# Kernel optimization log

Hardware: AMD Instinct MI355X
Metric: run time of the kernel (lower is better)

The kernel has to match this reference:

```python
import jax, jax.numpy as jnp
import numpy as np

NUM_HEAD = 16


def setup_inputs() -> dict:
    key = jax.random.key(0)
    k1, k2, k3 = jax.random.split(key, 3)
    E = 1024
    x = jax.random.normal(k1, (4, 2048, E), dtype=jnp.float32)
    W1 = jax.random.normal(k2, (E, 3 * E), dtype=jnp.float32) * 0.02
    b1 = jnp.zeros((3 * E,), dtype=jnp.float32)
    W2 = jax.random.normal(k3, (E, E), dtype=jnp.float32) * 0.02
    b2 = jnp.zeros((E,), dtype=jnp.float32)
    return {"x": x, "W1": W1, "b1": b1, "W2": W2, "b2": b2}


def reference(x, W1, b1, W2, b2):
    # Fused QKV projection: (n, s, 3E)
    h = x @ W1 + b1
    n, s, _ = h.shape
    # Split into heads FIRST (matches torch reshape), then transpose: (n, H, s, 3*d_head)
    h = h.reshape(n, s, NUM_HEAD, -1).transpose(0, 2, 1, 3)
    # Chunk last dim into q, k, v: each (n, H, s, d_head)
    q, k, v = jnp.split(h, 3, axis=-1)
    dk = jnp.asarray(v.shape[-1], x.dtype) ** 0.5
    # Naive full S x S attention (faithful to source)
    w = jnp.einsum("nhqd,nhkd->nhqk", q, k) / dk
    w = jax.nn.softmax(w, axis=-1)  # dropout1 is identity at eval
    att = jnp.einsum("nhqk,nhkd->nhqd", w, v)
    att = att.transpose(0, 2, 1, 3).reshape(n, s, -1)  # (n, s, E)
    return att @ W2 + b2  # dropout2 identity at eval
```

## Files before the change

kernel.cpp:

```cpp
#include <hip/hip_runtime.h>
#include <math.h>
#include <stdint.h>
#include <stddef.h>


#define SEQ    2048
#define NB     4
#define E_DIM  1024
#define N1     3072
#define M_TOK  8192
#define NHEAD  16
#define DHEAD  64

typedef __attribute__((ext_vector_type(4))) float    floatx4;
typedef __attribute__((ext_vector_type(8))) short    shortx8;
typedef __attribute__((ext_vector_type(4))) unsigned short ushortx4;

__device__ __forceinline__ unsigned short f2bf(float f) {
    union { float f; unsigned u; } v; v.f = f;
    unsigned r = (v.u + 0x7FFFu + ((v.u >> 16) & 1u)) >> 16;
    return (unsigned short)r;
}
__device__ __forceinline__ unsigned fbits(float f) {
    union { float f; unsigned u; } v; v.f = f; return v.u;
}
__device__ __forceinline__ float bitsf(unsigned u) {
    union { unsigned u; float f; } v; v.u = u; return v.f;
}

__device__ __forceinline__ void gl_lds16(const void* g, void* l) {
    __builtin_amdgcn_global_load_lds(
        (const __attribute__((address_space(1))) unsigned int*)g,
        (__attribute__((address_space(3))) unsigned int*)l, 16, 0, 0);
}

__global__ __launch_bounds__(256) void cvt_bf16(
    const float* __restrict__ in, unsigned short* __restrict__ out)
{
    const size_t i = ((size_t)blockIdx.x * 256 + threadIdx.x) * 8;
    float4 a = *(const float4*)(in + i);
    float4 b = *(const float4*)(in + i + 4);
    ushortx4 o0 = { f2bf(a.x), f2bf(a.y), f2bf(a.z), f2bf(a.w) };
    ushortx4 o1 = { f2bf(b.x), f2bf(b.y), f2bf(b.z), f2bf(b.w) };
    *(ushortx4*)(out + i)     = o0;
    *(ushortx4*)(out + i + 4) = o1;
}

__global__ __launch_bounds__(256) void cvt_transpose(
    const float* __restrict__ W, unsigned short* __restrict__ Wt, int K, int N)
{
    __shared__ unsigned short tile[32][33];
    const int tx = threadIdx.x, ty = threadIdx.y;
    const int n0 = blockIdx.x * 32, k0 = blockIdx.y * 32;
#pragma unroll
    for (int r = 0; r < 4; ++r) {
        const int k = ty + r * 8;
        tile[tx][k] = f2bf(W[(size_t)(k0 + k) * N + n0 + tx]);
    }
    __syncthreads();
#pragma unroll
    for (int r = 0; r < 4; ++r) {
        const int n = ty + r * 8;
        Wt[(size_t)(n0 + n) * K + k0 + tx] = tile[n][tx];
    }
}

template <bool OUT_BF16, bool FUSE>
__global__ __launch_bounds__(256) void gemm_bf16(
    const short* __restrict__ A, const short* __restrict__ Bt,
    const float* __restrict__ bias, void* __restrict__ Cout,
    unsigned short* __restrict__ Vt,
    int M, int N, int K)
{
    __shared__ short As[128 * 32];
    __shared__ short Bs[128 * 32];

    const int t    = threadIdx.x;
    const int lane = t & 63, w = t >> 6;
    const int quad = lane >> 4, l15 = lane & 15;
    const int bm = blockIdx.y * 128, bn = blockIdx.x * 128;
    const int m0w = (w >> 1) * 64, n0w = (w & 1) * 64;

    const int lrow = lane >> 2;
    const int lcol = (lane & 3) * 8;
    const short* Ag0 = A  + (size_t)(bm + (2 * w + 0) * 16 + lrow) * K + lcol;
    const short* Ag1 = A  + (size_t)(bm + (2 * w + 1) * 16 + lrow) * K + lcol;
    const short* Bg0 = Bt + (size_t)(bn + (2 * w + 0) * 16 + lrow) * K + lcol;
    const short* Bg1 = Bt + (size_t)(bn + (2 * w + 1) * 16 + lrow) * K + lcol;
    short* Al0 = As + (2 * w + 0) * 512;
    short* Al1 = As + (2 * w + 1) * 512;
    short* Bl0 = Bs + (2 * w + 0) * 512;
    short* Bl1 = Bs + (2 * w + 1) * 512;

    floatx4 acc[4][4];
#pragma unroll
    for (int i = 0; i < 4; ++i)
#pragma unroll
        for (int j = 0; j < 4; ++j) acc[i][j] = (floatx4)0.f;

    for (int k0 = 0; k0 < K; k0 += 32) {
        __syncthreads();
        gl_lds16(Ag0, Al0); gl_lds16(Ag1, Al1);
        gl_lds16(Bg0, Bl0); gl_lds16(Bg1, Bl1);
        Ag0 += 32; Ag1 += 32; Bg0 += 32; Bg1 += 32;
        __syncthreads();

        shortx8 af[4], bf[4];
#pragma unroll
        for (int mi = 0; mi < 4; ++mi)
            af[mi] = *(const shortx8*)(As + (m0w + mi * 16 + l15) * 32 + quad * 8);
#pragma unroll
        for (int ni = 0; ni < 4; ++ni)
            bf[ni] = *(const shortx8*)(Bs + (n0w + ni * 16 + l15) * 32 + quad * 8);
#pragma unroll
        for (int mi = 0; mi < 4; ++mi)
#pragma unroll
            for (int ni = 0; ni < 4; ++ni)
                acc[mi][ni] = __builtin_amdgcn_mfma_f32_16x16x32_bf16(
                    af[mi], bf[ni], acc[mi][ni], 0, 0, 0);
    }

    float bv[4];
#pragma unroll
    for (int ni = 0; ni < 4; ++ni) bv[ni] = bias[bn + n0w + ni * 16 + l15];

#pragma unroll
    for (int ni = 0; ni < 4; ++ni) {
        const int col   = bn + n0w + ni * 16 + l15;
        const int cm    = col % 192;
        const int vhead = col / 192;
#pragma unroll
        for (int mi = 0; mi < 4; ++mi) {
            const int row0 = bm + m0w + mi * 16 + quad * 4;
            float v[4];
#pragma unroll
            for (int r = 0; r < 4; ++r) v[r] = acc[mi][ni][r] + bv[ni];
            if (OUT_BF16) {
                if (FUSE && cm < DHEAD) {
#pragma unroll
                    for (int r = 0; r < 4; ++r) v[r] *= 0.125f;
                }
                unsigned short* H = (unsigned short*)Cout;
#pragma unroll
                for (int r = 0; r < 4; ++r)
                    H[(size_t)(row0 + r) * N + col] = f2bf(v[r]);
                if (FUSE && cm >= 2 * DHEAD) {
                    const int nb = row0 >> 11;
                    const int s  = row0 & 2047;
                    const int d  = cm - 2 * DHEAD;
                    ushortx4 pk = { f2bf(v[0]), f2bf(v[1]), f2bf(v[2]), f2bf(v[3]) };
                    *(ushortx4*)(Vt + ((size_t)(nb * NHEAD + vhead) * DHEAD + d) * SEQ + s) = pk;
                }
            } else {
                float* C = (float*)Cout;
#pragma unroll
                for (int r = 0; r < 4; ++r)
                    C[(size_t)(row0 + r) * N + col] = v[r];
            }
        }
    }
}

__global__ __launch_bounds__(256, 3) void attn_mfma(
    const short* __restrict__ h, const short* __restrict__ Vt,
    unsigned short* __restrict__ att)
{
    __shared__ short Ks[64 * 64];
    __shared__ short Vs[64 * 64];
    __shared__ short Pl[4][64 * 64];
    __shared__ float Ls[4][64];

    const int t    = threadIdx.x;
    const int lane = t & 63, w = t >> 6;
    const int quad = lane >> 4, l15 = lane & 15;
    const int r7   = l15 & 7;
    const int bh = blockIdx.x, n = bh >> 4, head = bh & 15;
    const int q0 = blockIdx.y * 256 + w * 64;

    const short* hQ  = h + (size_t)n * SEQ * N1 + head * (3 * DHEAD);
    const short* hK  = hQ + DHEAD;
    const short* Vtb = Vt + (size_t)bh * DHEAD * SEQ;

    const int srow = t >> 2;
    const int sc0  = (t & 3) * 2;
    const int sk   = srow & 7;
    const short* gK = hK  + (size_t)srow * N1  + sc0 * 8;
    const short* gV = Vtb + (size_t)srow * SEQ + sc0 * 8;
    short* lK0 = Ks + srow * 64 + ((sc0    ) ^ sk) * 8;
    short* lK1 = Ks + srow * 64 + ((sc0 + 1) ^ sk) * 8;
    short* lV0 = Vs + srow * 64 + ((sc0    ) ^ sk) * 8;
    short* lV1 = Vs + srow * 64 + ((sc0 + 1) ^ sk) * 8;

    shortx8 qf[4][2];
#pragma unroll
    for (int qt = 0; qt < 4; ++qt)
#pragma unroll
        for (int kt = 0; kt < 2; ++kt)
            qf[qt][kt] = *(const shortx8*)(hQ + (size_t)(q0 + qt * 16 + l15) * N1
                                           + kt * 32 + quad * 8);

    floatx4 O[4][4];
    float lsum[4];
#pragma unroll
    for (int mi = 0; mi < 4; ++mi) {
        lsum[mi] = 0.f;
#pragma unroll
        for (int nt = 0; nt < 4; ++nt) O[mi][nt] = (floatx4)0.f;
    }

    int4 ka = *(const int4*)gK, kb = *(const int4*)(gK + 8);
    int4 va = *(const int4*)gV, vb = *(const int4*)(gV + 8);

    short* Pw = Pl[w];

    for (int kv0 = 0; kv0 < SEQ; kv0 += 64) {
        __syncthreads();
        *(int4*)lK0 = ka;
        *(int4*)lK1 = kb;
        *(int4*)lV0 = va;
        *(int4*)lV1 = vb;
        __syncthreads();
        if (kv0 + 64 < SEQ) {
            const short* gKn = gK + (size_t)(kv0 + 64) * N1;
            const short* gVn = gV + (kv0 + 64);
            ka = *(const int4*)gKn; kb = *(const int4*)(gKn + 8);
            va = *(const int4*)gVn; vb = *(const int4*)(gVn + 8);
        }

#pragma unroll
        for (int kvt = 0; kvt < 4; ++kvt) {
            const short* krow = Ks + (kvt * 16 + l15) * 64;
            shortx8 kf0 = *(const shortx8*)(krow + ((quad ^ r7) * 8));
            shortx8 kf1 = *(const shortx8*)(krow + (((quad ^ r7) ^ 4) * 8));
            floatx4 s[4];
#pragma unroll
            for (int qt = 0; qt < 4; ++qt) {
                s[qt] = __builtin_amdgcn_mfma_f32_16x16x32_bf16(
                    kf0, qf[qt][0], (floatx4)0.f, 0, 0, 0);
                s[qt] = __builtin_amdgcn_mfma_f32_16x16x32_bf16(
                    kf1, qf[qt][1], s[qt], 0, 0, 0);
            }
#pragma unroll
            for (int qt = 0; qt < 4; ++qt) {
                const float p0 = __expf(s[qt][0]);
                const float p1 = __expf(s[qt][1]);
                const float p2 = __expf(s[qt][2]);
                const float p3 = __expf(s[qt][3]);
                const unsigned d01 = __builtin_amdgcn_perm(fbits(p1), fbits(p0), 0x07060302u);
                const unsigned d23 = __builtin_amdgcn_perm(fbits(p3), fbits(p2), 0x07060302u);
                lsum[qt] += bitsf(d01 << 16) + bitsf(d01 & 0xFFFF0000u)
                          + bitsf(d23 << 16) + bitsf(d23 & 0xFFFF0000u);
                uint2 pk = { d01, d23 };
                *(uint2*)(Pw + (qt * 16 + l15) * 64
                          + ((2 * kvt + (quad >> 1)) ^ r7) * 8 + (quad & 1) * 4) = pk;
            }
        }

#pragma unroll
        for (int kt2 = 0; kt2 < 2; ++kt2) {
            const int coff = (((kt2 * 4 + quad) ^ r7)) * 8;
            shortx8 pf[4], vf[4];
#pragma unroll
            for (int mi = 0; mi < 4; ++mi)
                pf[mi] = *(const shortx8*)(Pw + (mi * 16 + l15) * 64 +
                                           (((kt2 * 4 + quad) ^ r7)) * 8);
#pragma unroll
            for (int nt = 0; nt < 4; ++nt)
                vf[nt] = *(const shortx8*)(Vs + (nt * 16 + l15) * 64 + coff);
#pragma unroll
            for (int mi = 0; mi < 4; ++mi)
#pragma unroll
                for (int nt = 0; nt < 4; ++nt)
                    O[mi][nt] = __builtin_amdgcn_mfma_f32_16x16x32_bf16(
                        pf[mi], vf[nt], O[mi][nt], 0, 0, 0);
        }
    }

#pragma unroll
    for (int qt = 0; qt < 4; ++qt) {
        lsum[qt] += __shfl_xor(lsum[qt], 16);
        lsum[qt] += __shfl_xor(lsum[qt], 32);
    }
    if (quad == 0) {
#pragma unroll
        for (int qt = 0; qt < 4; ++qt) Ls[w][qt * 16 + l15] = lsum[qt];
    }

#pragma unroll
    for (int mi = 0; mi < 4; ++mi)
#pragma unroll
        for (int r = 0; r < 4; ++r) {
            const int   ql  = mi * 16 + quad * 4 + r;
            const float inv = 1.f / Ls[w][ql];
            const size_t row = (size_t)n * SEQ + q0 + ql;
#pragma unroll
            for (int nt = 0; nt < 4; ++nt)
                att[row * E_DIM + head * DHEAD + nt * 16 + l15] =
                    f2bf(O[mi][nt][r] * inv);
        }
}

extern "C" void kernel_launch(void* const* d_in, const int* in_sizes, int n_in,
                              void* d_out, int out_size, void* d_ws, size_t ws_size,
                              hipStream_t stream)
{
    const float* x  = (const float*)d_in[0];
    const float* W1 = (const float*)d_in[1];
    const float* b1 = (const float*)d_in[2];
    const float* W2 = (const float*)d_in[3];
    const float* b2 = (const float*)d_in[4];
    float* out = (float*)d_out;

    char* ws = (char*)d_ws;
    unsigned short* x_bf  = (unsigned short*)(ws);
    unsigned short* W1t   = (unsigned short*)(ws + (16u << 20));
    unsigned short* W2t   = (unsigned short*)(ws + (22u << 20));
    unsigned short* h_bf  = (unsigned short*)(ws + (24u << 20));
    unsigned short* attb  = (unsigned short*)(ws + (72u << 20));
    unsigned short* Vtw   = (unsigned short*)(ws + (88u << 20));

    cvt_bf16<<<dim3((M_TOK * E_DIM) / (256 * 8)), 256, 0, stream>>>(x, x_bf);
    cvt_transpose<<<dim3(N1 / 32, E_DIM / 32), dim3(32, 8), 0, stream>>>(W1, W1t, E_DIM, N1);
    cvt_transpose<<<dim3(E_DIM / 32, E_DIM / 32), dim3(32, 8), 0, stream>>>(W2, W2t, E_DIM, E_DIM);

    gemm_bf16<true, true><<<dim3(N1 / 128, M_TOK / 128), 256, 0, stream>>>(
        (const short*)x_bf, (const short*)W1t, b1, h_bf, Vtw, M_TOK, N1, E_DIM);

    attn_mfma<<<dim3(NB * NHEAD, SEQ / 256), 256, 0, stream>>>(
        (const short*)h_bf, (const short*)Vtw, attb);

    gemm_bf16<false, false><<<dim3(E_DIM / 128, M_TOK / 128), 256, 0, stream>>>(
        (const short*)attb, (const short*)W2t, b2, out, nullptr, M_TOK, E_DIM, E_DIM);
}
```

Before: 301.3 us.

## Shrink attention blocks to two waves and use native exp2 with folded scale

The attention kernel now runs 128-thread blocks covering 128 queries instead of 256. This doubles the grid and halves the LDS used per block, but each thread now stages four 16-byte K and V chunks instead of two. Softmax exponentials switch to the hardware exp2 builtin, with log2(e) folded into the Q pre-scale in the QKV GEMM epilogue, which removes a multiply per exp. The trade-off is that K/V tile staging is now shared by fewer waves, so each wave does more global-to-LDS traffic, and register pressure rises from the larger prefetch buffers.

```diff
diff --git a/kernel.cpp b/kernel.cpp
--- a/kernel.cpp
+++ b/kernel.cpp
@@ -15,6 +15,12 @@
 typedef __attribute__((ext_vector_type(4))) float    floatx4;
 typedef __attribute__((ext_vector_type(8))) short    shortx8;
 typedef __attribute__((ext_vector_type(4))) unsigned short ushortx4;
+
+#if __has_builtin(__builtin_amdgcn_exp2f)
+#define EXP2(x) __builtin_amdgcn_exp2f(x)
+#else
+#define EXP2(x) __expf((x) * 0.6931471805599453f)
+#endif
 
 __device__ __forceinline__ unsigned short f2bf(float f) {
     union { float f; unsigned u; } v; v.f = f;
@@ -138,7 +144,7 @@
             if (OUT_BF16) {
                 if (FUSE && cm < DHEAD) {
 #pragma unroll
-                    for (int r = 0; r < 4; ++r) v[r] *= 0.125f;
+                    for (int r = 0; r < 4; ++r) v[r] *= 0.18033688011112042f;
                 }
                 unsigned short* H = (unsigned short*)Cout;
 #pragma unroll
@@ -161,35 +167,33 @@
     }
 }
 
-__global__ __launch_bounds__(256, 3) void attn_mfma(
+__global__ __launch_bounds__(128, 2) void attn_mfma(
     const short* __restrict__ h, const short* __restrict__ Vt,
     unsigned short* __restrict__ att)
 {
     __shared__ short Ks[64 * 64];
     __shared__ short Vs[64 * 64];
-    __shared__ short Pl[4][64 * 64];
-    __shared__ float Ls[4][64];
+    __shared__ short Pl[2][64 * 64];
+    __shared__ float Ls[2][64];
 
     const int t    = threadIdx.x;
     const int lane = t & 63, w = t >> 6;
     const int quad = lane >> 4, l15 = lane & 15;
     const int r7   = l15 & 7;
     const int bh = blockIdx.x, n = bh >> 4, head = bh & 15;
-    const int q0 = blockIdx.y * 256 + w * 64;
+    const int q0 = blockIdx.y * 128 + w * 64;
 
     const short* hQ  = h + (size_t)n * SEQ * N1 + head * (3 * DHEAD);
     const short* hK  = hQ + DHEAD;
     const short* Vtb = Vt + (size_t)bh * DHEAD * SEQ;
 
-    const int srow = t >> 2;
-    const int sc0  = (t & 3) * 2;
+    const int srow = t >> 1;
+    const int sc0  = (t & 1) * 4;
     const int sk   = srow & 7;
     const short* gK = hK  + (size_t)srow * N1  + sc0 * 8;
     const short* gV = Vtb + (size_t)srow * SEQ + sc0 * 8;
-    short* lK0 = Ks + srow * 64 + ((sc0    ) ^ sk) * 8;
-    short* lK1 = Ks + srow * 64 + ((sc0 + 1) ^ sk) * 8;
-    short* lV0 = Vs + srow * 64 + ((sc0    ) ^ sk) * 8;
-    short* lV1 = Vs + srow * 64 + ((sc0 + 1) ^ sk) * 8;
+    short* lKr = Ks + srow * 64;
+    short* lVr = Vs + srow * 64;
 
     shortx8 qf[4][2];
 #pragma unroll
@@ -208,23 +212,31 @@
         for (int nt = 0; nt < 4; ++nt) O[mi][nt] = (floatx4)0.f;
     }
 
-    int4 ka = *(const int4*)gK, kb = *(const int4*)(gK + 8);
-    int4 va = *(const int4*)gV, vb = *(const int4*)(gV + 8);
+    int4 kr[4], vr[4];
+#pragma unroll
+    for (int i = 0; i < 4; ++i) {
+        kr[i] = *(const int4*)(gK + i * 8);
+        vr[i] = *(const int4*)(gV + i * 8);
+    }
 
     short* Pw = Pl[w];
 
     for (int kv0 = 0; kv0 < SEQ; kv0 += 64) {
         __syncthreads();
-        *(int4*)lK0 = ka;
-        *(int4*)lK1 = kb;
-        *(int4*)lV0 = va;
-        *(int4*)lV1 = vb;
+#pragma unroll
+        for (int i = 0; i < 4; ++i) {
+            *(int4*)(lKr + ((sc0 + i) ^ sk) * 8) = kr[i];
+            *(int4*)(lVr + ((sc0 + i) ^ sk) * 8) = vr[i];
+        }
         __syncthreads();
         if (kv0 + 64 < SEQ) {
             const short* gKn = gK + (size_t)(kv0 + 64) * N1;
             const short* gVn = gV + (kv0 + 64);
-            ka = *(const int4*)gKn; kb = *(const int4*)(gKn + 8);
-            va = *(const int4*)gVn; vb = *(const int4*)(gVn + 8);
+#pragma unroll
+            for (int i = 0; i < 4; ++i) {
+                kr[i] = *(const int4*)(gKn + i * 8);
+                vr[i] = *(const int4*)(gVn + i * 8);
+            }
         }
 
 #pragma unroll
@@ -242,10 +254,10 @@
             }
 #pragma unroll
             for (int qt = 0; qt < 4; ++qt) {
-                const float p0 = __expf(s[qt][0]);
-                const float p1 = __expf(s[qt][1]);
-                const float p2 = __expf(s[qt][2]);
-                const float p3 = __expf(s[qt][3]);
+                const float p0 = EXP2(s[qt][0]);
+                const float p1 = EXP2(s[qt][1]);
+                const float p2 = EXP2(s[qt][2]);
+                const float p3 = EXP2(s[qt][3]);
                 const unsigned d01 = __builtin_amdgcn_perm(fbits(p1), fbits(p0), 0x07060302u);
                 const unsigned d23 = __builtin_amdgcn_perm(fbits(p3), fbits(p2), 0x07060302u);
                 lsum[qt] += bitsf(d01 << 16) + bitsf(d01 & 0xFFFF0000u)
@@ -262,8 +274,7 @@
             shortx8 pf[4], vf[4];
 #pragma unroll
             for (int mi = 0; mi < 4; ++mi)
-                pf[mi] = *(const shortx8*)(Pw + (mi * 16 + l15) * 64 +
-                                           (((kt2 * 4 + quad) ^ r7)) * 8);
+                pf[mi] = *(const shortx8*)(Pw + (mi * 16 + l15) * 64 + coff);
 #pragma unroll
             for (int nt = 0; nt < 4; ++nt)
                 vf[nt] = *(const shortx8*)(Vs + (nt * 16 + l15) * 64 + coff);
@@ -326,7 +337,7 @@
     gemm_bf16<true, true><<<dim3(N1 / 128, M_TOK / 128), 256, 0, stream>>>(
         (const short*)x_bf, (const short*)W1t, b1, h_bf, Vtw, M_TOK, N1, E_DIM);
 
-    attn_mfma<<<dim3(NB * NHEAD, SEQ / 256), 256, 0, stream>>>(
+    attn_mfma<<<dim3(NB * NHEAD, SEQ / 128), 128, 0, stream>>>(
         (const short*)h_bf, (const short*)Vtw, attb);
 
     gemm_bf16<false, false><<<dim3(E_DIM / 128, M_TOK / 128), 256, 0, stream>>>(
```

Result: slower. 371.4 us (+23.2%).

## Split attention work across wave pairs and use exp2 with folded log2e scale

Applied to the files above, without the earlier changes.

Each 64-query tile is now shared by two waves: each wave computes scores for half of the key tile and accumulates half of the output columns, exchanging probabilities through shared LDS with an added barrier. Blocks cover 128 queries, so the grid doubles, and launch bounds allow four blocks per CU thanks to the smaller P buffer and accumulator footprint. The Q scale now folds in log2(e) so the kernel can call the hardware exp2 instead of __expf. The trade-off is an extra __syncthreads per KV tile and redundant K/V loads per block.

```diff
diff --git a/kernel.cpp b/kernel.cpp
--- a/kernel.cpp
+++ b/kernel.cpp
@@ -15,6 +15,12 @@
 typedef __attribute__((ext_vector_type(4))) float    floatx4;
 typedef __attribute__((ext_vector_type(8))) short    shortx8;
 typedef __attribute__((ext_vector_type(4))) unsigned short ushortx4;
+
+#if __has_builtin(__builtin_amdgcn_exp2f)
+#define EXP2(x) __builtin_amdgcn_exp2f(x)
+#else
+#define EXP2(x) __expf((x) * 0.6931471805599453f)
+#endif
 
 __device__ __forceinline__ unsigned short f2bf(float f) {
     union { float f; unsigned u; } v; v.f = f;
@@ -138,7 +144,7 @@
             if (OUT_BF16) {
                 if (FUSE && cm < DHEAD) {
 #pragma unroll
-                    for (int r = 0; r < 4; ++r) v[r] *= 0.125f;
+                    for (int r = 0; r < 4; ++r) v[r] *= 0.18033688011112042f;
                 }
                 unsigned short* H = (unsigned short*)Cout;
 #pragma unroll
@@ -161,21 +167,22 @@
     }
 }
 
-__global__ __launch_bounds__(256, 3) void attn_mfma(
+__global__ __launch_bounds__(256, 4) void attn_mfma(
     const short* __restrict__ h, const short* __restrict__ Vt,
     unsigned short* __restrict__ att)
 {
     __shared__ short Ks[64 * 64];
     __shared__ short Vs[64 * 64];
-    __shared__ short Pl[4][64 * 64];
-    __shared__ float Ls[4][64];
+    __shared__ short Pl[2][64 * 64];
+    __shared__ float Ls2[2][2][64];
 
     const int t    = threadIdx.x;
     const int lane = t & 63, w = t >> 6;
+    const int p    = w >> 1, e = w & 1;
     const int quad = lane >> 4, l15 = lane & 15;
     const int r7   = l15 & 7;
     const int bh = blockIdx.x, n = bh >> 4, head = bh & 15;
-    const int q0 = blockIdx.y * 256 + w * 64;
+    const int q0 = blockIdx.y * 128 + p * 64;
 
     const short* hQ  = h + (size_t)n * SEQ * N1 + head * (3 * DHEAD);
     const short* hK  = hQ + DHEAD;
@@ -199,19 +206,19 @@
             qf[qt][kt] = *(const shortx8*)(hQ + (size_t)(q0 + qt * 16 + l15) * N1
                                            + kt * 32 + quad * 8);
 
-    floatx4 O[4][4];
+    floatx4 O[4][2];
     float lsum[4];
 #pragma unroll
     for (int mi = 0; mi < 4; ++mi) {
         lsum[mi] = 0.f;
 #pragma unroll
-        for (int nt = 0; nt < 4; ++nt) O[mi][nt] = (floatx4)0.f;
+        for (int nt = 0; nt < 2; ++nt) O[mi][nt] = (floatx4)0.f;
     }
 
     int4 ka = *(const int4*)gK, kb = *(const int4*)(gK + 8);
     int4 va = *(const int4*)gV, vb = *(const int4*)(gV + 8);
 
-    short* Pw = Pl[w];
+    short* Pp = Pl[p];
 
     for (int kv0 = 0; kv0 < SEQ; kv0 += 64) {
         __syncthreads();
@@ -228,10 +235,11 @@
         }
 
 #pragma unroll
-        for (int kvt = 0; kvt < 4; ++kvt) {
-            const short* krow = Ks + (kvt * 16 + l15) * 64;
+        for (int ii = 0; ii < 2; ++ii) {
+            const int si = 2 * e + ii;
+            const short* krow = Ks + (si * 16 + l15) * 64;
             shortx8 kf0 = *(const shortx8*)(krow + ((quad ^ r7) * 8));
-            shortx8 kf1 = *(const shortx8*)(krow + (((quad ^ r7) ^ 4) * 8));
+            shortx8 kf1 = *(const shortx8*)(krow + (((quad ^ 4) ^ r7) * 8));
             floatx4 s[4];
 #pragma unroll
             for (int qt = 0; qt < 4; ++qt) {
@@ -242,35 +250,35 @@
             }
 #pragma unroll
             for (int qt = 0; qt < 4; ++qt) {
-                const float p0 = __expf(s[qt][0]);
-                const float p1 = __expf(s[qt][1]);
-                const float p2 = __expf(s[qt][2]);
-                const float p3 = __expf(s[qt][3]);
+                const float p0 = EXP2(s[qt][0]);
+                const float p1 = EXP2(s[qt][1]);
+                const float p2 = EXP2(s[qt][2]);
+                const float p3 = EXP2(s[qt][3]);
                 const unsigned d01 = __builtin_amdgcn_perm(fbits(p1), fbits(p0), 0x07060302u);
                 const unsigned d23 = __builtin_amdgcn_perm(fbits(p3), fbits(p2), 0x07060302u);
                 lsum[qt] += bitsf(d01 << 16) + bitsf(d01 & 0xFFFF0000u)
                           + bitsf(d23 << 16) + bitsf(d23 & 0xFFFF0000u);
                 uint2 pk = { d01, d23 };
-                *(uint2*)(Pw + (qt * 16 + l15) * 64
-                          + ((2 * kvt + (quad >> 1)) ^ r7) * 8 + (quad & 1) * 4) = pk;
+                *(uint2*)(Pp + (qt * 16 + l15) * 64
+                          + ((si * 2 + (quad >> 1)) ^ r7) * 8 + (quad & 1) * 4) = pk;
             }
         }
+        __syncthreads();
 
 #pragma unroll
         for (int kt2 = 0; kt2 < 2; ++kt2) {
-            const int coff = (((kt2 * 4 + quad) ^ r7)) * 8;
-            shortx8 pf[4], vf[4];
+            const int coff = ((kt2 * 4 + quad) ^ r7) * 8;
+            shortx8 pf[4], vf[2];
 #pragma unroll
             for (int mi = 0; mi < 4; ++mi)
-                pf[mi] = *(const shortx8*)(Pw + (mi * 16 + l15) * 64 +
-                                           (((kt2 * 4 + quad) ^ r7)) * 8);
-#pragma unroll
-            for (int nt = 0; nt < 4; ++nt)
-                vf[nt] = *(const shortx8*)(Vs + (nt * 16 + l15) * 64 + coff);
+                pf[mi] = *(const shortx8*)(Pp + (mi * 16 + l15) * 64 + coff);
+#pragma unroll
+            for (int nt = 0; nt < 2; ++nt)
+                vf[nt] = *(const shortx8*)(Vs + ((2 * e + nt) * 16 + l15) * 64 + coff);
 #pragma unroll
             for (int mi = 0; mi < 4; ++mi)
 #pragma unroll
-                for (int nt = 0; nt < 4; ++nt)
+                for (int nt = 0; nt < 2; ++nt)
                     O[mi][nt] = __builtin_amdgcn_mfma_f32_16x16x32_bf16(
                         pf[mi], vf[nt], O[mi][nt], 0, 0, 0);
         }
@@ -283,19 +291,20 @@
     }
     if (quad == 0) {
 #pragma unroll
-        for (int qt = 0; qt < 4; ++qt) Ls[w][qt * 16 + l15] = lsum[qt];
-    }
+        for (int qt = 0; qt < 4; ++qt) Ls2[p][e][qt * 16 + l15] = lsum[qt];
+    }
+    __syncthreads();
 
 #pragma unroll
     for (int mi = 0; mi < 4; ++mi)
 #pragma unroll
         for (int r = 0; r < 4; ++r) {
             const int   ql  = mi * 16 + quad * 4 + r;
-            const float inv = 1.f / Ls[w][ql];
+            const float inv = 1.f / (Ls2[p][0][ql] + Ls2[p][1][ql]);
             const size_t row = (size_t)n * SEQ + q0 + ql;
 #pragma unroll
-            for (int nt = 0; nt < 4; ++nt)
-                att[row * E_DIM + head * DHEAD + nt * 16 + l15] =
+            for (int nt = 0; nt < 2; ++nt)
+                att[row * E_DIM + head * DHEAD + (2 * e + nt) * 16 + l15] =
                     f2bf(O[mi][nt][r] * inv);
         }
 }
@@ -326,7 +335,7 @@
     gemm_bf16<true, true><<<dim3(N1 / 128, M_TOK / 128), 256, 0, stream>>>(
         (const short*)x_bf, (const short*)W1t, b1, h_bf, Vtw, M_TOK, N1, E_DIM);
 
-    attn_mfma<<<dim3(NB * NHEAD, SEQ / 256), 256, 0, stream>>>(
+    attn_mfma<<<dim3(NB * NHEAD, SEQ / 128), 256, 0, stream>>>(
         (const short*)h_bf, (const short*)Vtw, attb);
 
     gemm_bf16<false, false><<<dim3(E_DIM / 128, M_TOK / 128), 256, 0, stream>>>(
```

New measurement: 297.4 us. About the same (-1.3%).
